# Kernel optimization log

Measured on AMD Instinct MI355X. Metric: run time of the kernel, lower is better.

## Reference

```python
import jax, jax.numpy as jnp
import numpy as np

# camera / raster constants
N = 10000            # gaussians
W = 256
H = 256
FX = 200.0
FY = 200.0
TILE = 16
NTX = W // TILE
NTY = H // TILE
NT = NTX * NTY       # 256 tiles
P = TILE * TILE      # 256 pixels per tile
K = 256              # max gaussians kept per tile
NEAR = 0.3
MAGIC = 1.2          # frustum expansion factor from project_culling
LP = 0.3 / (FX * FX) # low-pass filter added to 2D covariance diagonal


def quat_to_rot(q):
    w, x, y, z = q[:, 0], q[:, 1], q[:, 2], q[:, 3]
    r0 = jnp.stack([1 - 2 * (y * y + z * z), 2 * (x * y - w * z), 2 * (x * z + w * y)], -1)
    r1 = jnp.stack([2 * (x * y + w * z), 1 - 2 * (x * x + z * z), 2 * (y * z - w * x)], -1)
    r2 = jnp.stack([2 * (x * z - w * y), 2 * (y * z + w * x), 1 - 2 * (x * x + y * y)], -1)
    return jnp.stack([r0, r1, r2], axis=1)  # [N,3,3]


def splat_forward(pos, rgb, opacity, quaternion, scale, w2c_r, w2c_t):
    # ---- project + frustum cull (global_culling) ----
    q = quaternion / jnp.linalg.norm(quaternion, axis=-1, keepdims=True)
    R = quat_to_rot(q)
    sigma = jnp.exp(scale)                               # normalize_scale
    cov3d = jnp.einsum('nij,nj,nkj->nik', R, sigma * sigma, R)
    p_cam = pos @ w2c_r.T + w2c_t                        # [N,3]
    x, y, z = p_cam[:, 0], p_cam[:, 1], p_cam[:, 2]
    zc = jnp.maximum(z, 1e-6)
    half_w = W * MAGIC / 2 / FX
    half_h = H * MAGIC / 2 / FY
    mean2d = jnp.stack([x / zc, y / zc], -1)             # camera-plane coords
    in_frustum = (z > NEAR) & (jnp.abs(mean2d[:, 0]) < half_w) & (jnp.abs(mean2d[:, 1]) < half_h)
    iz = 1.0 / zc
    zero = jnp.zeros_like(iz)
    J = jnp.stack([jnp.stack([iz, zero, -x * iz * iz], -1),
                   jnp.stack([zero, iz, -y * iz * iz], -1)], axis=1)  # [N,2,3]
    cov_cam = jnp.einsum('ij,njk,lk->nil', w2c_r, cov3d, w2c_r)
    cov2d = jnp.einsum('nij,njk,nlk->nil', J, cov_cam, J)            # [N,2,2]
    a = cov2d[:, 0, 0] + LP
    c = cov2d[:, 1, 1] + LP
    b = cov2d[:, 0, 1]

    # ---- per-tile culling + fixed-K binning (calc_tile_list / gather_gaussians) ----
    cx = (jnp.arange(NTX) * TILE + TILE / 2 - W / 2) / FX
    cy = (jnp.arange(NTY) * TILE + TILE / 2 - H / 2) / FY
    centers = jnp.stack(jnp.meshgrid(cx, cy, indexing='xy'), -1).reshape(NT, 2)  # [NT,2] (ty-major)
    tile_half_diag = 0.5 * jnp.sqrt((TILE / FX) ** 2 + (TILE / FY) ** 2)
    mid = 0.5 * (a + c)
    sigma_max = jnp.sqrt(jnp.maximum(mid + jnp.sqrt(jnp.maximum((0.5 * (a - c)) ** 2 + b * b, 0.0)), 1e-12))
    dist = jnp.linalg.norm(centers[:, None, :] - mean2d[None, :, :], axis=-1)   # [NT,N]
    valid = in_frustum[None, :] & (dist <= (3.0 * sigma_max + tile_half_diag)[None, :])
    score = jnp.where(valid, -dist, -1e10)
    vals, idx = jax.lax.top_k(score, K)                                          # [NT,K]
    valid_k = vals > -1e9

    mean_g = mean2d[idx]                     # [NT,K,2]
    z_g = z[idx]
    a_g, b_g, c_g = a[idx], b[idx], c[idx]
    opa_g = jax.nn.sigmoid(opacity)[idx]
    rgb_g = jax.nn.sigmoid(rgb)[idx]         # [NT,K,3]

    # ---- depth sort within each tile ----
    order = jnp.argsort(jnp.where(valid_k, z_g, jnp.inf), axis=-1)
    def srt(arr):
        o = order.reshape(order.shape + (1,) * (arr.ndim - 2))
        return jnp.take_along_axis(arr, o, axis=1)
    mean_s, a_s, b_s, c_s = srt(mean_g), srt(a_g), srt(b_g), srt(c_g)
    opa_s, rgb_s = srt(opa_g), srt(rgb_g)
    valid_s = srt(valid_k).astype(pos.dtype)

    # ---- per-pixel front-to-back alpha compositing (draw) ----
    px = ((jnp.arange(W) + 0.5 - W / 2) / FX).reshape(NTX, TILE)
    py = ((jnp.arange(H) + 0.5 - H / 2) / FY).reshape(NTY, TILE)
    U = jnp.broadcast_to(px[None, :, None, :], (NTY, NTX, TILE, TILE)).reshape(NT, P)
    V = jnp.broadcast_to(py[:, None, :, None], (NTY, NTX, TILE, TILE)).reshape(NT, P)
    dx = U[:, :, None] - mean_s[:, None, :, 0]          # [NT,P,K]
    dy = V[:, :, None] - mean_s[:, None, :, 1]
    det = jnp.maximum(a_s * c_s - b_s * b_s, 1e-12)[:, None, :]
    maha = (c_s[:, None, :] * dx * dx - 2.0 * b_s[:, None, :] * dx * dy + a_s[:, None, :] * dy * dy) / det
    alpha = jnp.clip(opa_s[:, None, :] * jnp.exp(-0.5 * maha), 0.0, 0.99) * valid_s[:, None, :]
    trans = jnp.cumprod(1.0 - alpha, axis=-1)
    texc = jnp.concatenate([jnp.ones_like(trans[..., :1]), trans[..., :-1]], axis=-1)
    color = jnp.einsum('tpk,tkc->tpc', alpha * texc, rgb_s)  # [NT,P,3]
    img = color.reshape(NTY, NTX, TILE, TILE, 3).transpose(0, 2, 1, 3, 4).reshape(H, W, 3)
    return jnp.clip(img, 0.0, 1.0)


def setup_inputs() -> dict:
    key = jax.random.key(0)
    ks = jax.random.split(key, 6)
    zpos = jax.random.uniform(ks[0], (N,), minval=2.0, maxval=6.0)
    uv = jax.random.uniform(ks[1], (N, 2), minval=-0.6, maxval=0.6)
    pos = jnp.concatenate([uv * zpos[:, None], zpos[:, None]], axis=-1)
    rgb = jax.random.normal(ks[2], (N, 3))              # pre-sigmoid logits
    opacity = jax.random.normal(ks[3], (N,)) + 1.5      # sigmoid -> ~0.8 like init_opacity
    quaternion = jax.random.normal(ks[4], (N, 4))
    scale = 0.2 * jax.random.normal(ks[5], (N, 3)) - 4.5  # exp -> ~0.01 world sigma
    w2c_r = jnp.eye(3, dtype=jnp.float32)
    w2c_t = jnp.zeros((3,), dtype=jnp.float32)
    return {"pos": pos, "rgb": rgb, "opacity": opacity, "quaternion": quaternion,
            "scale": scale, "w2c_r": w2c_r, "w2c_t": w2c_t}


def reference(pos, rgb, opacity, quaternion, scale, w2c_r, w2c_t):
    return splat_forward(pos, rgb, opacity, quaternion, scale, w2c_r, w2c_t)
```

## Files before the change

kernel.cpp:

```cpp
#include <hip/hip_runtime.h>
#include <math.h>

namespace {
constexpr int W = 256, H = 256, TILE = 16, NTX = 16, NT = 256, K = 256;
constexpr float FX = 200.0f, FY = 200.0f, NEARP = 0.3f, MAGIC = 1.2f;
constexpr float LP = 0.3f / (FX * FX);
constexpr float HALF_W = W * MAGIC / 2.0f / FX;
constexpr float HALF_H = H * MAGIC / 2.0f / FY;
constexpr float THDIAG = 0.05656854249492381f;
constexpr int CAP = 1024;
constexpr int N_PAD = 10240;
constexpr int BT = 1024;
constexpr int NB_MAX = 64;
constexpr int SEG = 256;
constexpr int NSPL = 16;
constexpr size_t A_OFF  = 0;
constexpr size_t B_OFF  = A_OFF + (size_t)N_PAD * 16;
constexpr size_t C_OFF  = B_OFF + (size_t)N_PAD * 16;
constexpr size_t SL_OFF = C_OFF + (size_t)N_PAD * 16;
constexpr size_t LD_OFF = SL_OFF + (size_t)NT * NB_MAX * 4;
constexpr size_t LZ_OFF = LD_OFF + (size_t)NT * NB_MAX * SEG * 8;
constexpr size_t WS_FULL = LZ_OFF + (size_t)NT * NB_MAX * SEG * 8;
}

struct Pre { float mx, my, z, a, b, c, radius; };

__device__ inline Pre preprocess(int g, const float* __restrict__ pos,
                                 const float* __restrict__ quat,
                                 const float* __restrict__ scl,
                                 const float* __restrict__ w2cr,
                                 const float* __restrict__ w2ct) {
  float p0 = pos[3*g+0], p1 = pos[3*g+1], p2 = pos[3*g+2];
  float qw = quat[4*g+0], qx = quat[4*g+1], qy = quat[4*g+2], qz = quat[4*g+3];
  float inv = 1.0f / sqrtf(qw*qw + qx*qx + qy*qy + qz*qz);
  qw *= inv; qx *= inv; qy *= inv; qz *= inv;
  float r00 = 1.f-2.f*(qy*qy+qz*qz), r01 = 2.f*(qx*qy-qw*qz), r02 = 2.f*(qx*qz+qw*qy);
  float r10 = 2.f*(qx*qy+qw*qz), r11 = 1.f-2.f*(qx*qx+qz*qz), r12 = 2.f*(qy*qz-qw*qx);
  float r20 = 2.f*(qx*qz-qw*qy), r21 = 2.f*(qy*qz+qw*qx), r22 = 1.f-2.f*(qx*qx+qy*qy);
  float e0 = __expf(scl[3*g+0]); float s0 = e0*e0;
  float e1 = __expf(scl[3*g+1]); float s1 = e1*e1;
  float e2 = __expf(scl[3*g+2]); float s2 = e2*e2;
  float C00 = r00*r00*s0 + r01*r01*s1 + r02*r02*s2;
  float C01 = r00*r10*s0 + r01*r11*s1 + r02*r12*s2;
  float C02 = r00*r20*s0 + r01*r21*s1 + r02*r22*s2;
  float C11 = r10*r10*s0 + r11*r11*s1 + r12*r12*s2;
  float C12 = r10*r20*s0 + r11*r21*s1 + r12*r22*s2;
  float C22 = r20*r20*s0 + r21*r21*s1 + r22*r22*s2;
  float w00=w2cr[0],w01=w2cr[1],w02=w2cr[2];
  float w10=w2cr[3],w11=w2cr[4],w12=w2cr[5];
  float w20=w2cr[6],w21=w2cr[7],w22=w2cr[8];
  float x = w00*p0 + w01*p1 + w02*p2 + w2ct[0];
  float y = w10*p0 + w11*p1 + w12*p2 + w2ct[1];
  float z = w20*p0 + w21*p1 + w22*p2 + w2ct[2];
  float m00 = w00*C00 + w01*C01 + w02*C02;
  float m01 = w00*C01 + w01*C11 + w02*C12;
  float m02 = w00*C02 + w01*C12 + w02*C22;
  float m10 = w10*C00 + w11*C01 + w12*C02;
  float m11 = w10*C01 + w11*C11 + w12*C12;
  float m12 = w10*C02 + w11*C12 + w12*C22;
  float m20 = w20*C00 + w21*C01 + w22*C02;
  float m21 = w20*C01 + w21*C11 + w22*C12;
  float m22 = w20*C02 + w21*C12 + w22*C22;
  float v00 = m00*w00 + m01*w01 + m02*w02;
  float v01 = m00*w10 + m01*w11 + m02*w12;
  float v02 = m00*w20 + m01*w21 + m02*w22;
  float v10 = m10*w00 + m11*w01 + m12*w02;
  float v11 = m10*w10 + m11*w11 + m12*w12;
  float v12 = m10*w20 + m11*w21 + m12*w22;
  float v20 = m20*w00 + m21*w01 + m22*w02;
  float v21 = m20*w10 + m21*w11 + m22*w12;
  float v22 = m20*w20 + m21*w21 + m22*w22;
  float zc = fmaxf(z, 1e-6f);
  float iz = 1.0f / zc;
  float mx = x * iz, my = y * iz;
  float iz2 = iz * iz;
  float jx = -x * iz2, jy = -y * iz2;
  float a00 = iz*v00 + jx*v20, a01 = iz*v01 + jx*v21, a02 = iz*v02 + jx*v22;
  float a10 = iz*v10 + jy*v20, a11 = iz*v11 + jy*v21, a12 = iz*v12 + jy*v22;
  float A  = a00*iz + a02*jx + LP;
  float Bv = a01*iz + a02*jy;
  float Cv = a11*iz + a12*jy + LP;
  float mid = 0.5f*(A + Cv);
  float hh  = 0.5f*(A - Cv);
  float disc = fmaxf(hh*hh + Bv*Bv, 0.0f);
  float smax = sqrtf(fmaxf(mid + sqrtf(disc), 1e-12f));
  bool infr = (z > NEARP) && (fabsf(mx) < HALF_W) && (fabsf(my) < HALF_H);
  Pre r;
  r.mx = mx; r.my = my; r.z = z; r.a = A; r.b = Bv; r.c = Cv;
  r.radius = infr ? (3.0f * smax + THDIAG) : -1.0f;
  return r;
}


template <bool BIN>
__global__ __launch_bounds__(256)
void pre_bin(const float* __restrict__ pos, const float* __restrict__ rgb,
             const float* __restrict__ opac, const float* __restrict__ quat,
             const float* __restrict__ scl, const float* __restrict__ w2cr,
             const float* __restrict__ w2ct,
             float4* __restrict__ pa, float4* __restrict__ pb,
             float4* __restrict__ pc, int* __restrict__ seglen,
             unsigned long long* __restrict__ listd,
             unsigned long long* __restrict__ listz, int n) {
  __shared__ int s_tc[NT];
  const int tid = (int)threadIdx.x;
  const int blk = (int)blockIdx.x;
  if (BIN) {
    if (tid < NT) s_tc[tid] = 0;
    __syncthreads();
  }
  const int g = blk * 256 + tid;
  if (g < n) {
    Pre p = preprocess(g, pos, quat, scl, w2cr, w2ct);
    float det = fmaxf(p.a * p.c - p.b * p.b, 1e-12f);
    float ivd = 1.0f / det;
    float lopa = -__logf(1.0f + __expf(-opac[g]));
    pa[g] = make_float4(p.mx, p.my, p.radius, p.z);
    pb[g] = make_float4(-0.5f * ivd * p.c, ivd * p.b, -0.5f * ivd * p.a, lopa);
    pc[g] = make_float4(1.0f / (1.0f + __expf(-rgb[3*g+0])),
                        1.0f / (1.0f + __expf(-rgb[3*g+1])),
                        1.0f / (1.0f + __expf(-rgb[3*g+2])), 0.0f);
    if (BIN && p.radius >= 0.0f) {
      float r = p.radius;
      int txlo = max(0,     (int)floorf(((p.mx - r) * FX + 120.0f) * 0.0625f));
      int txhi = min(NTX-1, (int)ceilf (((p.mx + r) * FX + 120.0f) * 0.0625f));
      int tylo = max(0,     (int)floorf(((p.my - r) * FY + 120.0f) * 0.0625f));
      int tyhi = min(NTX-1, (int)ceilf (((p.my + r) * FY + 120.0f) * 0.0625f));
      unsigned long long gbits = (unsigned int)g;
      for (int ty = tylo; ty <= tyhi; ++ty) {
        float cy = (ty * TILE + TILE * 0.5f - H * 0.5f) / FY;
        float ddy = cy - p.my;
        for (int tx = txlo; tx <= txhi; ++tx) {
          float cx = (tx * TILE + TILE * 0.5f - W * 0.5f) / FX;
          float ddx = cx - p.mx;
          float dist = sqrtf(ddx * ddx + ddy * ddy);
          if (dist <= r) {
            int t = ty * NTX + tx;
            int slot = atomicAdd(&s_tc[t], 1);
            size_t idx = ((size_t)t * NB_MAX + blk) * SEG + slot;
            listd[idx] = ((unsigned long long)__float_as_uint(dist) << 32) | gbits;
            listz[idx] = ((unsigned long long)__float_as_uint(p.z)  << 32) | gbits;
          }
        }
      }
    }
  }
  if (BIN) {
    __syncthreads();
    if (tid < NT) seglen[(size_t)tid * NB_MAX + blk] = s_tc[tid];
  }
}


__device__ inline void hsort1(unsigned long long* key, int M) {
  const int tid = (int)threadIdx.x;
  __syncthreads();
  unsigned long long e = (tid < M) ? key[tid] : ~0ull;
  for (int k = 2; k <= M; k <<= 1) {
    for (int j = k >> 1; j >= 64; j >>= 1) {
      __syncthreads();
      if (tid < M) key[tid] = e;
      __syncthreads();
      if (tid < M) {
        unsigned long long p = key[tid ^ j];
        bool takeMin = (((tid & j) == 0) == ((tid & k) == 0));
        e = ((p < e) == takeMin) ? p : e;
      }
    }
    int j0 = ((k >> 1) < 32) ? (k >> 1) : 32;
    for (int j = j0; j >= 1; j >>= 1) {
      unsigned long long p = __shfl_xor(e, j, 64);
      bool takeMin = (((tid & j) == 0) == ((tid & k) == 0));
      e = ((p < e) == takeMin) ? p : e;
    }
  }
  __syncthreads();
  if (tid < M) key[tid] = e;
  __syncthreads();
}


__device__ inline void tail16(
    const float4* __restrict__ pa, const float4* __restrict__ pb,
    const float4* __restrict__ pc, float* __restrict__ out,
    unsigned long long* s_zkey, int* s_rank,
    float4* s_p0, float4* s_p1, float* s_cb, float4* s_part,
    int cnt2, int tx, int ty) {
  const int tid = (int)threadIdx.x;
  {
    const int e = tid & 255;
    const int q = tid >> 8;
    const int rchunk = (cnt2 + 3) >> 2;
    if (e < cnt2) {
      unsigned long long mykey = s_zkey[e];
      int jlo = q * rchunk;
      int jhi = min(cnt2, jlo + rchunk);
      int partial = 0;
      for (int j = jlo; j < jhi; ++j)
        partial += (s_zkey[j] < mykey) ? 1 : 0;
      if (partial) atomicAdd(&s_rank[e], partial);
    }
  }
  __syncthreads();
  if (tid < cnt2) {
    int g = (int)(s_zkey[tid] & 0xffffffffu);
    int r = s_rank[tid];
    float4 A = pa[g], B = pb[g], C = pc[g];
    s_p0[r] = make_float4(A.x, A.y, B.x, B.y);
    s_p1[r] = make_float4(B.z, B.w, C.x, C.y);
    s_cb[r] = C.z;
  }
  __syncthreads();

  const int p6  = tid & 63;
  const int q16 = tid >> 6;
  const int prow0 = p6 >> 4;
  const int pcol  = p6 & 15;
  const float u  = ((float)(tx * TILE + pcol) + 0.5f - W * 0.5f) / FX;
  const float v0 = ((float)(ty * TILE + prow0 +  0) + 0.5f - H * 0.5f) / FY;
  const float v1 = ((float)(ty * TILE + prow0 +  4) + 0.5f - H * 0.5f) / FY;
  const float v2 = ((float)(ty * TILE + prow0 +  8) + 0.5f - H * 0.5f) / FY;
  const float v3 = ((float)(ty * TILE + prow0 + 12) + 0.5f - H * 0.5f) / FY;
  const int chunk = (cnt2 + NSPL - 1) / NSPL;
  const int k0 = q16 * chunk;
  const int k1 = min(cnt2, k0 + chunk);
  float T0 = 1.0f, r0 = 0.0f, g0 = 0.0f, b0 = 0.0f;
  float T1 = 1.0f, r1 = 0.0f, g1 = 0.0f, b1 = 0.0f;
  float T2 = 1.0f, r2 = 0.0f, g2 = 0.0f, b2 = 0.0f;
  float T3 = 1.0f, r3 = 0.0f, g3 = 0.0f, b3 = 0.0f;
  for (int k2 = k0; k2 < k1; ++k2) {
    float4 P0 = s_p0[k2];
    float4 P1 = s_p1[k2];
    float cb = s_cb[k2];
    float dx = u - P0.x;
    float s  = fmaf(P0.z * dx, dx, P1.y);
    float bd = P0.w * dx;
    {
      float dy = v0 - P0.y;
      float m  = fmaf(fmaf(P1.x, dy, bd), dy, s);
      float a  = fminf(__expf(m), 0.99f);
      float w  = a * T0;
      r0 = fmaf(w, P1.z, r0); g0 = fmaf(w, P1.w, g0); b0 = fmaf(w, cb, b0);
      T0 = fmaf(-a, T0, T0);
    }
    {
      float dy = v1 - P0.y;
      float m  = fmaf(fmaf(P1.x, dy, bd), dy, s);
      float a  = fminf(__expf(m), 0.99f);
      float w  = a * T1;
      r1 = fmaf(w, P1.z, r1); g1 = fmaf(w, P1.w, g1); b1 = fmaf(w, cb, b1);
      T1 = fmaf(-a, T1, T1);
    }
    {
      float dy = v2 - P0.y;
      float m  = fmaf(fmaf(P1.x, dy, bd), dy, s);
      float a  = fminf(__expf(m), 0.99f);
      float w  = a * T2;
      r2 = fmaf(w, P1.z, r2); g2 = fmaf(w, P1.w, g2); b2 = fmaf(w, cb, b2);
      T2 = fmaf(-a, T2, T2);
    }
    {
      float dy = v3 - P0.y;
      float m  = fmaf(fmaf(P1.x, dy, bd), dy, s);
      float a  = fminf(__expf(m), 0.99f);
      float w  = a * T3;
      r3 = fmaf(w, P1.z, r3); g3 = fmaf(w, P1.w, g3); b3 = fmaf(w, cb, b3);
      T3 = fmaf(-a, T3, T3);
    }
  }
  s_part[q16 * 256 + p6 +   0] = make_float4(r0, g0, b0, T0);
  s_part[q16 * 256 + p6 +  64] = make_float4(r1, g1, b1, T1);
  s_part[q16 * 256 + p6 + 128] = make_float4(r2, g2, b2, T2);
  s_part[q16 * 256 + p6 + 192] = make_float4(r3, g3, b3, T3);
  __syncthreads();

  if (tid < 256) {
    float4 P = s_part[(NSPL - 1) * 256 + tid];
    float r = P.x, g = P.y, b = P.z;
    #pragma unroll
    for (int q = NSPL - 2; q >= 0; --q) {
      float4 Q = s_part[q * 256 + tid];
      r = fmaf(Q.w, r, Q.x);
      g = fmaf(Q.w, g, Q.y);
      b = fmaf(Q.w, b, Q.z);
    }
    const int p6o = tid & 63;
    const int sub = tid >> 6;
    const int prow = (p6o >> 4) + 4 * sub;
    const int pcol2 = p6o & 15;
    const int row = ty * TILE + prow;
    const int col = tx * TILE + pcol2;
    const int o = (row * W + col) * 3;
    out[o+0] = fminf(fmaxf(r, 0.0f), 1.0f);
    out[o+1] = fminf(fmaxf(g, 0.0f), 1.0f);
    out[o+2] = fminf(fmaxf(b, 0.0f), 1.0f);
  }
}


__global__ __launch_bounds__(BT)
void render_list(const float4* __restrict__ pa, const float4* __restrict__ pb,
                 const float4* __restrict__ pc, const int* __restrict__ seglen,
                 const unsigned long long* __restrict__ listd,
                 const unsigned long long* __restrict__ listz,
                 float* __restrict__ out, int nb) {
  __shared__ unsigned long long s_zkey[CAP];
  __shared__ unsigned long long s_dkey[CAP];
  __shared__ int s_off[NB_MAX + 1];
  __shared__ int s_rank[K];
  __shared__ float4 s_p0[K];
  __shared__ float4 s_p1[K];
  __shared__ float  s_cb[K];
  __shared__ float4 s_part[NSPL * 256];

  const int t  = (int)blockIdx.x;
  const int tx = t % NTX;
  const int ty = t / NTX;
  const int tid = (int)threadIdx.x;

  if (tid < K) s_rank[tid] = 0;
  if (tid < 64) {
    int v = (tid < nb) ? seglen[(size_t)t * NB_MAX + tid] : 0;
    #pragma unroll
    for (int d = 1; d < 64; d <<= 1) {
      int u2 = __shfl_up(v, d, 64);
      if (tid >= d) v += u2;
    }
    if (tid == 0) s_off[0] = 0;
    if (tid < nb) s_off[tid + 1] = v;
  }
  __syncthreads();
  int cnt = min(s_off[nb], CAP);

  for (int i = tid; i < cnt; i += BT) {
    int lo = 0, hi = nb;
    while (hi - lo > 1) {
      int mid = (lo + hi) >> 1;
      if (s_off[mid] <= i) lo = mid; else hi = mid;
    }
    size_t src = ((size_t)t * NB_MAX + lo) * SEG + (size_t)(i - s_off[lo]);
    s_zkey[i] = listz[src];
  }
  __syncthreads();
  int cnt2 = cnt;

  if (cnt > K) {
    for (int i = tid; i < cnt; i += BT) {
      int lo = 0, hi = nb;
      while (hi - lo > 1) {
        int mid = (lo + hi) >> 1;
        if (s_off[mid] <= i) lo = mid; else hi = mid;
      }
      size_t src = ((size_t)t * NB_MAX + lo) * SEG + (size_t)(i - s_off[lo]);
      s_dkey[i] = listd[src];
    }
    int M = 512; while (M < cnt) M <<= 1;
    for (int i = cnt + tid; i < M; i += BT) s_dkey[i] = ~0ull;
    hsort1(s_dkey, M);
    if (tid < K) {
      int g = (int)(s_dkey[tid] & 0xffffffffu);
      s_zkey[tid] = ((unsigned long long)__float_as_uint(pa[g].w) << 32) |
                    (unsigned int)g;
    }
    __syncthreads();
    cnt2 = K;
  }

  tail16(pa, pb, pc, out, s_zkey, s_rank, s_p0, s_p1, s_cb, s_part, cnt2, tx, ty);
}


__global__ __launch_bounds__(BT)
void render_scan(const float4* __restrict__ pa, const float4* __restrict__ pb,
                 const float4* __restrict__ pc, float* __restrict__ out, int n) {
  __shared__ unsigned long long s_zkey[CAP];
  __shared__ unsigned long long s_dkey[CAP];
  __shared__ int s_rank[K];
  __shared__ float4 s_p0[K];
  __shared__ float4 s_p1[K];
  __shared__ float  s_cb[K];
  __shared__ float4 s_part[NSPL * 256];
  __shared__ int s_cnt;

  const int t  = (int)blockIdx.x;
  const int tx = t % NTX;
  const int ty = t / NTX;
  const int tid = (int)threadIdx.x;
  const int lane = tid & 63;
  const float cxc = (tx * TILE + TILE * 0.5f - W * 0.5f) / FX;
  const float cyc = (ty * TILE + TILE * 0.5f - H * 0.5f) / FY;

  if (tid == 0) s_cnt = 0;
  if (tid < K) s_rank[tid] = 0;
  __syncthreads();

  for (int g = tid; g < n; g += BT) {
    float4 v = pa[g];
    float ddx = cxc - v.x, ddy = cyc - v.y;
    float dist = sqrtf(ddx * ddx + ddy * ddy);
    bool hit = (v.z >= 0.0f) && (dist <= v.z);
    unsigned long long m = __ballot(hit);
    if (m) {
      int leader = __ffsll((long long)m) - 1;
      int base = 0;
      if (lane == leader) base = atomicAdd(&s_cnt, __popcll(m));
      base = __shfl(base, leader, 64);
      if (hit) {
        int slot = base + __popcll(m & ((1ull << lane) - 1ull));
        if (slot < CAP) {
          s_dkey[slot] = ((unsigned long long)__float_as_uint(dist) << 32) |
                         (unsigned int)g;
          s_zkey[slot] = ((unsigned long long)__float_as_uint(v.w) << 32) |
                         (unsigned int)g;
        }
      }
    }
  }
  __syncthreads();
  int cnt = min(s_cnt, CAP);
  int cnt2 = cnt;

  if (cnt > K) {
    int M = 512; while (M < cnt) M <<= 1;
    for (int i = cnt + tid; i < M; i += BT) s_dkey[i] = ~0ull;
    hsort1(s_dkey, M);
    if (tid < K) {
      int g = (int)(s_dkey[tid] & 0xffffffffu);
      s_zkey[tid] = ((unsigned long long)__float_as_uint(pa[g].w) << 32) |
                    (unsigned int)g;
    }
    __syncthreads();
    cnt2 = K;
  }

  tail16(pa, pb, pc, out, s_zkey, s_rank, s_p0, s_p1, s_cb, s_part, cnt2, tx, ty);
}

extern "C" void kernel_launch(void* const* d_in, const int* in_sizes, int n_in,
                              void* d_out, int out_size, void* d_ws, size_t ws_size,
                              hipStream_t stream) {
  const float* pos  = (const float*)d_in[0];
  const float* rgb  = (const float*)d_in[1];
  const float* opac = (const float*)d_in[2];
  const float* quat = (const float*)d_in[3];
  const float* scl  = (const float*)d_in[4];
  const float* w2cr = (const float*)d_in[5];
  const float* w2ct = (const float*)d_in[6];
  float* out = (float*)d_out;
  const int n = in_sizes[0] / 3;
  const int nb = (n + 255) / 256;

  char* ws = (char*)d_ws;
  float4* pa = (float4*)(ws + A_OFF);
  float4* pb = (float4*)(ws + B_OFF);
  float4* pc = (float4*)(ws + C_OFF);
  int* seglen = (int*)(ws + SL_OFF);
  unsigned long long* listd = (unsigned long long*)(ws + LD_OFF);
  unsigned long long* listz = (unsigned long long*)(ws + LZ_OFF);

  if (ws_size >= WS_FULL && nb <= NB_MAX) {
    pre_bin<true><<<nb, 256, 0, stream>>>(
        pos, rgb, opac, quat, scl, w2cr, w2ct, pa, pb, pc, seglen, listd, listz, n);
    render_list<<<NT, BT, 0, stream>>>(pa, pb, pc, seglen, listd, listz, out, nb);
  } else {
    pre_bin<false><<<nb, 256, 0, stream>>>(
        pos, rgb, opac, quat, scl, w2cr, w2ct, pa, pb, pc, seglen, listd, listz, n);
    render_scan<<<NT, BT, 0, stream>>>(pa, pb, pc, out, n);
  }
}
```

Measured before the change: 21.17 us.

## Spread preprocess/binning over 256 small blocks to fill more CUs

The binning kernel now launches 256 blocks of 64 threads (about 40 gaussians each) instead of 40 blocks of 256 threads. The goal is to occupy more compute units in the preprocess stage. The render kernel's segment prefix scan grows from 64 to 256 entries, using a two-level wave scan through shared memory. The fallback path is split into a separate non-binning kernel. This adds more segment metadata per tile and a longer binary search in the gather step.

Result: no change. 21.36 us (+0.9%).

```diff
diff --git a/kernel.cpp b/kernel.cpp
--- a/kernel.cpp
+++ b/kernel.cpp
@@ -11,16 +11,17 @@
 constexpr int CAP = 1024;
 constexpr int N_PAD = 10240;
 constexpr int BT = 1024;
-constexpr int NB_MAX = 64;
-constexpr int SEG = 256;
+constexpr int NBB = 256;
+constexpr int BPRE = 64;
+constexpr int SEG = 64;
 constexpr int NSPL = 16;
 constexpr size_t A_OFF  = 0;
 constexpr size_t B_OFF  = A_OFF + (size_t)N_PAD * 16;
 constexpr size_t C_OFF  = B_OFF + (size_t)N_PAD * 16;
 constexpr size_t SL_OFF = C_OFF + (size_t)N_PAD * 16;
-constexpr size_t LD_OFF = SL_OFF + (size_t)NT * NB_MAX * 4;
-constexpr size_t LZ_OFF = LD_OFF + (size_t)NT * NB_MAX * SEG * 8;
-constexpr size_t WS_FULL = LZ_OFF + (size_t)NT * NB_MAX * SEG * 8;
+constexpr size_t LD_OFF = SL_OFF + (size_t)NT * NBB * 4;
+constexpr size_t LZ_OFF = LD_OFF + (size_t)NT * NBB * SEG * 8;
+constexpr size_t WS_FULL = LZ_OFF + (size_t)NT * NBB * SEG * 8;
 }
 
 struct Pre { float mx, my, z, a, b, c, radius; };
@@ -91,9 +92,22 @@
   return r;
 }
 
-
-template <bool BIN>
-__global__ __launch_bounds__(256)
+__device__ inline void store_params(int g, const float* __restrict__ rgb,
+                                    const float* __restrict__ opac, Pre p,
+                                    float4* __restrict__ pa, float4* __restrict__ pb,
+                                    float4* __restrict__ pc) {
+  float det = fmaxf(p.a * p.c - p.b * p.b, 1e-12f);
+  float ivd = 1.0f / det;
+  float lopa = -__logf(1.0f + __expf(-opac[g]));
+  pa[g] = make_float4(p.mx, p.my, p.radius, p.z);
+  pb[g] = make_float4(-0.5f * ivd * p.c, ivd * p.b, -0.5f * ivd * p.a, lopa);
+  pc[g] = make_float4(1.0f / (1.0f + __expf(-rgb[3*g+0])),
+                      1.0f / (1.0f + __expf(-rgb[3*g+1])),
+                      1.0f / (1.0f + __expf(-rgb[3*g+2])), 0.0f);
+}
+
+
+__global__ __launch_bounds__(BPRE)
 void pre_bin(const float* __restrict__ pos, const float* __restrict__ rgb,
              const float* __restrict__ opac, const float* __restrict__ quat,
              const float* __restrict__ scl, const float* __restrict__ w2cr,
@@ -101,26 +115,17 @@
              float4* __restrict__ pa, float4* __restrict__ pb,
              float4* __restrict__ pc, int* __restrict__ seglen,
              unsigned long long* __restrict__ listd,
-             unsigned long long* __restrict__ listz, int n) {
+             unsigned long long* __restrict__ listz, int n, int gpb) {
   __shared__ int s_tc[NT];
   const int tid = (int)threadIdx.x;
   const int blk = (int)blockIdx.x;
-  if (BIN) {
-    if (tid < NT) s_tc[tid] = 0;
-    __syncthreads();
-  }
-  const int g = blk * 256 + tid;
-  if (g < n) {
+  for (int t = tid; t < NT; t += BPRE) s_tc[t] = 0;
+  __syncthreads();
+  const int g = blk * gpb + tid;
+  if (tid < gpb && g < n) {
     Pre p = preprocess(g, pos, quat, scl, w2cr, w2ct);
-    float det = fmaxf(p.a * p.c - p.b * p.b, 1e-12f);
-    float ivd = 1.0f / det;
-    float lopa = -__logf(1.0f + __expf(-opac[g]));
-    pa[g] = make_float4(p.mx, p.my, p.radius, p.z);
-    pb[g] = make_float4(-0.5f * ivd * p.c, ivd * p.b, -0.5f * ivd * p.a, lopa);
-    pc[g] = make_float4(1.0f / (1.0f + __expf(-rgb[3*g+0])),
-                        1.0f / (1.0f + __expf(-rgb[3*g+1])),
-                        1.0f / (1.0f + __expf(-rgb[3*g+2])), 0.0f);
-    if (BIN && p.radius >= 0.0f) {
+    store_params(g, rgb, opac, p, pa, pb, pc);
+    if (p.radius >= 0.0f) {
       float r = p.radius;
       int txlo = max(0,     (int)floorf(((p.mx - r) * FX + 120.0f) * 0.0625f));
       int txhi = min(NTX-1, (int)ceilf (((p.mx + r) * FX + 120.0f) * 0.0625f));
@@ -137,7 +142,7 @@
           if (dist <= r) {
             int t = ty * NTX + tx;
             int slot = atomicAdd(&s_tc[t], 1);
-            size_t idx = ((size_t)t * NB_MAX + blk) * SEG + slot;
+            size_t idx = ((size_t)t * NBB + blk) * SEG + slot;
             listd[idx] = ((unsigned long long)__float_as_uint(dist) << 32) | gbits;
             listz[idx] = ((unsigned long long)__float_as_uint(p.z)  << 32) | gbits;
           }
@@ -145,10 +150,22 @@
       }
     }
   }
-  if (BIN) {
-    __syncthreads();
-    if (tid < NT) seglen[(size_t)tid * NB_MAX + blk] = s_tc[tid];
-  }
+  __syncthreads();
+  for (int t = tid; t < NT; t += BPRE)
+    seglen[(size_t)t * NBB + blk] = s_tc[t];
+}
+
+__global__ __launch_bounds__(256)
+void pre_only(const float* __restrict__ pos, const float* __restrict__ rgb,
+              const float* __restrict__ opac, const float* __restrict__ quat,
+              const float* __restrict__ scl, const float* __restrict__ w2cr,
+              const float* __restrict__ w2ct,
+              float4* __restrict__ pa, float4* __restrict__ pb,
+              float4* __restrict__ pc, int n) {
+  int g = blockIdx.x * 256 + (int)threadIdx.x;
+  if (g >= n) return;
+  Pre p = preprocess(g, pos, quat, scl, w2cr, w2ct);
+  store_params(g, rgb, opac, p, pa, pb, pc);
 }
 
 
@@ -303,10 +320,11 @@
                  const float4* __restrict__ pc, const int* __restrict__ seglen,
                  const unsigned long long* __restrict__ listd,
                  const unsigned long long* __restrict__ listz,
-                 float* __restrict__ out, int nb) {
+                 float* __restrict__ out) {
   __shared__ unsigned long long s_zkey[CAP];
   __shared__ unsigned long long s_dkey[CAP];
-  __shared__ int s_off[NB_MAX + 1];
+  __shared__ int s_off[NBB + 1];
+  __shared__ int s_wsum[4];
   __shared__ int s_rank[K];
   __shared__ float4 s_p0[K];
   __shared__ float4 s_p1[K];
@@ -317,28 +335,39 @@
   const int tx = t % NTX;
   const int ty = t / NTX;
   const int tid = (int)threadIdx.x;
+  const int lane = tid & 63;
 
   if (tid < K) s_rank[tid] = 0;
-  if (tid < 64) {
-    int v = (tid < nb) ? seglen[(size_t)t * NB_MAX + tid] : 0;
+  int v = 0;
+  if (tid < NBB) {
+    v = seglen[(size_t)t * NBB + tid];
     #pragma unroll
     for (int d = 1; d < 64; d <<= 1) {
       int u2 = __shfl_up(v, d, 64);
-      if (tid >= d) v += u2;
-    }
+      if (lane >= d) v += u2;
+    }
+    if (lane == 63) s_wsum[tid >> 6] = v;
+  }
+  __syncthreads();
+  if (tid < NBB) {
+    int w = tid >> 6;
+    int add = 0;
+    #pragma unroll
+    for (int w2 = 0; w2 < 3; ++w2)
+      if (w2 < w) add += s_wsum[w2];
+    s_off[tid + 1] = v + add;
     if (tid == 0) s_off[0] = 0;
-    if (tid < nb) s_off[tid + 1] = v;
-  }
-  __syncthreads();
-  int cnt = min(s_off[nb], CAP);
+  }
+  __syncthreads();
+  int cnt = min(s_off[NBB], CAP);
 
   for (int i = tid; i < cnt; i += BT) {
-    int lo = 0, hi = nb;
+    int lo = 0, hi = NBB;
     while (hi - lo > 1) {
       int mid = (lo + hi) >> 1;
       if (s_off[mid] <= i) lo = mid; else hi = mid;
     }
-    size_t src = ((size_t)t * NB_MAX + lo) * SEG + (size_t)(i - s_off[lo]);
+    size_t src = ((size_t)t * NBB + lo) * SEG + (size_t)(i - s_off[lo]);
     s_zkey[i] = listz[src];
   }
   __syncthreads();
@@ -346,12 +375,12 @@
 
   if (cnt > K) {
     for (int i = tid; i < cnt; i += BT) {
-      int lo = 0, hi = nb;
+      int lo = 0, hi = NBB;
       while (hi - lo > 1) {
         int mid = (lo + hi) >> 1;
         if (s_off[mid] <= i) lo = mid; else hi = mid;
       }
-      size_t src = ((size_t)t * NB_MAX + lo) * SEG + (size_t)(i - s_off[lo]);
+      size_t src = ((size_t)t * NBB + lo) * SEG + (size_t)(i - s_off[lo]);
       s_dkey[i] = listd[src];
     }
     int M = 512; while (M < cnt) M <<= 1;
@@ -448,7 +477,7 @@
   const float* w2ct = (const float*)d_in[6];
   float* out = (float*)d_out;
   const int n = in_sizes[0] / 3;
-  const int nb = (n + 255) / 256;
+  const int gpb = (n + NBB - 1) / NBB;
 
   char* ws = (char*)d_ws;
   float4* pa = (float4*)(ws + A_OFF);
@@ -458,13 +487,14 @@
   unsigned long long* listd = (unsigned long long*)(ws + LD_OFF);
   unsigned long long* listz = (unsigned long long*)(ws + LZ_OFF);
 
-  if (ws_size >= WS_FULL && nb <= NB_MAX) {
-    pre_bin<true><<<nb, 256, 0, stream>>>(
-        pos, rgb, opac, quat, scl, w2cr, w2ct, pa, pb, pc, seglen, listd, listz, n);
-    render_list<<<NT, BT, 0, stream>>>(pa, pb, pc, seglen, listd, listz, out, nb);
+  if (ws_size >= WS_FULL && gpb <= BPRE && gpb <= SEG) {
+    pre_bin<<<NBB, BPRE, 0, stream>>>(
+        pos, rgb, opac, quat, scl, w2cr, w2ct, pa, pb, pc, seglen, listd, listz,
+        n, gpb);
+    render_list<<<NT, BT, 0, stream>>>(pa, pb, pc, seglen, listd, listz, out);
   } else {
-    pre_bin<false><<<nb, 256, 0, stream>>>(
-        pos, rgb, opac, quat, scl, w2cr, w2ct, pa, pb, pc, seglen, listd, listz, n);
+    pre_only<<<(n + 255) / 256, 256, 0, stream>>>(
+        pos, rgb, opac, quat, scl, w2cr, w2ct, pa, pb, pc, n);
     render_scan<<<NT, BT, 0, stream>>>(pa, pb, pc, out, n);
   }
 }
```

## Halve render block size to 512 threads and use shared-memory bitonic sort

Applied to the files above, without the earlier changes.

Render blocks shrink from 1024 to 512 threads, and the compositing split drops from 16 to 8 depth chunks per pixel group, so each thread composites more Gaussians. The register-and-shuffle hybrid bitonic sort is replaced by a plain shared-memory bitonic sort that loops over elements with a stride of the block size. The rank-counting pass changes from 4 to 2 partitions. This is meant to lower per-block sync cost and allow more resident blocks, at the cost of fewer threads per tile and more barriers in the sort.

Measured after the change: 22.73 us. 7.4% more time.

```diff
diff --git a/kernel.cpp b/kernel.cpp
--- a/kernel.cpp
+++ b/kernel.cpp
@@ -10,10 +10,10 @@
 constexpr float THDIAG = 0.05656854249492381f;
 constexpr int CAP = 1024;
 constexpr int N_PAD = 10240;
-constexpr int BT = 1024;
+constexpr int BT = 512;
 constexpr int NB_MAX = 64;
 constexpr int SEG = 256;
-constexpr int NSPL = 16;
+constexpr int NSPL = 8;
 constexpr size_t A_OFF  = 0;
 constexpr size_t B_OFF  = A_OFF + (size_t)N_PAD * 16;
 constexpr size_t C_OFF  = B_OFF + (size_t)N_PAD * 16;
@@ -152,35 +152,26 @@
 }
 
 
-__device__ inline void hsort1(unsigned long long* key, int M) {
+__device__ inline void bsort(unsigned long long* key, int M) {
   const int tid = (int)threadIdx.x;
-  __syncthreads();
-  unsigned long long e = (tid < M) ? key[tid] : ~0ull;
   for (int k = 2; k <= M; k <<= 1) {
-    for (int j = k >> 1; j >= 64; j >>= 1) {
+    for (int j = k >> 1; j > 0; j >>= 1) {
       __syncthreads();
-      if (tid < M) key[tid] = e;
-      __syncthreads();
-      if (tid < M) {
-        unsigned long long p = key[tid ^ j];
-        bool takeMin = (((tid & j) == 0) == ((tid & k) == 0));
-        e = ((p < e) == takeMin) ? p : e;
+      for (int i = tid; i < M; i += BT) {
+        int ixj = i ^ j;
+        if (ixj > i) {
+          unsigned long long a = key[i], b = key[ixj];
+          bool up = ((i & k) == 0);
+          if (up ? (a > b) : (a < b)) { key[i] = b; key[ixj] = a; }
+        }
       }
     }
-    int j0 = ((k >> 1) < 32) ? (k >> 1) : 32;
-    for (int j = j0; j >= 1; j >>= 1) {
-      unsigned long long p = __shfl_xor(e, j, 64);
-      bool takeMin = (((tid & j) == 0) == ((tid & k) == 0));
-      e = ((p < e) == takeMin) ? p : e;
-    }
-  }
-  __syncthreads();
-  if (tid < M) key[tid] = e;
-  __syncthreads();
-}
-
-
-__device__ inline void tail16(
+  }
+  __syncthreads();
+}
+
+
+__device__ inline void tail8(
     const float4* __restrict__ pa, const float4* __restrict__ pb,
     const float4* __restrict__ pc, float* __restrict__ out,
     unsigned long long* s_zkey, int* s_rank,
@@ -190,7 +181,7 @@
   {
     const int e = tid & 255;
     const int q = tid >> 8;
-    const int rchunk = (cnt2 + 3) >> 2;
+    const int rchunk = (cnt2 + 1) >> 1;
     if (e < cnt2) {
       unsigned long long mykey = s_zkey[e];
       int jlo = q * rchunk;
@@ -212,8 +203,8 @@
   }
   __syncthreads();
 
-  const int p6  = tid & 63;
-  const int q16 = tid >> 6;
+  const int p6 = tid & 63;
+  const int q8 = tid >> 6;
   const int prow0 = p6 >> 4;
   const int pcol  = p6 & 15;
   const float u  = ((float)(tx * TILE + pcol) + 0.5f - W * 0.5f) / FX;
@@ -222,7 +213,7 @@
   const float v2 = ((float)(ty * TILE + prow0 +  8) + 0.5f - H * 0.5f) / FY;
   const float v3 = ((float)(ty * TILE + prow0 + 12) + 0.5f - H * 0.5f) / FY;
   const int chunk = (cnt2 + NSPL - 1) / NSPL;
-  const int k0 = q16 * chunk;
+  const int k0 = q8 * chunk;
   const int k1 = min(cnt2, k0 + chunk);
   float T0 = 1.0f, r0 = 0.0f, g0 = 0.0f, b0 = 0.0f;
   float T1 = 1.0f, r1 = 0.0f, g1 = 0.0f, b1 = 0.0f;
@@ -268,10 +259,10 @@
       T3 = fmaf(-a, T3, T3);
     }
   }
-  s_part[q16 * 256 + p6 +   0] = make_float4(r0, g0, b0, T0);
-  s_part[q16 * 256 + p6 +  64] = make_float4(r1, g1, b1, T1);
-  s_part[q16 * 256 + p6 + 128] = make_float4(r2, g2, b2, T2);
-  s_part[q16 * 256 + p6 + 192] = make_float4(r3, g3, b3, T3);
+  s_part[q8 * 256 + p6 +   0] = make_float4(r0, g0, b0, T0);
+  s_part[q8 * 256 + p6 +  64] = make_float4(r1, g1, b1, T1);
+  s_part[q8 * 256 + p6 + 128] = make_float4(r2, g2, b2, T2);
+  s_part[q8 * 256 + p6 + 192] = make_float4(r3, g3, b3, T3);
   __syncthreads();
 
   if (tid < 256) {
@@ -356,7 +347,8 @@
     }
     int M = 512; while (M < cnt) M <<= 1;
     for (int i = cnt + tid; i < M; i += BT) s_dkey[i] = ~0ull;
-    hsort1(s_dkey, M);
+    __syncthreads();
+    bsort(s_dkey, M);
     if (tid < K) {
       int g = (int)(s_dkey[tid] & 0xffffffffu);
       s_zkey[tid] = ((unsigned long long)__float_as_uint(pa[g].w) << 32) |
@@ -366,7 +358,7 @@
     cnt2 = K;
   }
 
-  tail16(pa, pb, pc, out, s_zkey, s_rank, s_p0, s_p1, s_cb, s_part, cnt2, tx, ty);
+  tail8(pa, pb, pc, out, s_zkey, s_rank, s_p0, s_p1, s_cb, s_part, cnt2, tx, ty);
 }
 
 
@@ -423,7 +415,8 @@
   if (cnt > K) {
     int M = 512; while (M < cnt) M <<= 1;
     for (int i = cnt + tid; i < M; i += BT) s_dkey[i] = ~0ull;
-    hsort1(s_dkey, M);
+    __syncthreads();
+    bsort(s_dkey, M);
     if (tid < K) {
       int g = (int)(s_dkey[tid] & 0xffffffffu);
       s_zkey[tid] = ((unsigned long long)__float_as_uint(pa[g].w) << 32) |
@@ -433,7 +426,7 @@
     cnt2 = K;
   }
 
-  tail16(pa, pb, pc, out, s_zkey, s_rank, s_p0, s_p1, s_cb, s_part, cnt2, tx, ty);
+  tail8(pa, pb, pc, out, s_zkey, s_rank, s_p0, s_p1, s_cb, s_part, cnt2, tx, ty);
 }
 
 extern "C" void kernel_launch(void* const* d_in, const int* in_sizes, int n_in,
```
